# Performance work log

Hardware: AMD Instinct MI355X
Metric: run time of the kernel (lower is better)

The kernel has to match this reference:

```python
import jax, jax.numpy as jnp
import numpy as np

# snntorch default surrogate: ATan with alpha=2.0
@jax.custom_vjp
def spike_fn(x):
    return (x > 0).astype(x.dtype)

def _spike_fwd(x):
    return spike_fn(x), x

def _spike_bwd(x, g):
    alpha = 2.0
    return (g * (alpha / 2.0) / (1.0 + (jnp.pi / 2.0 * alpha * x) ** 2),)

spike_fn.defvjp(_spike_fwd, _spike_bwd)

B, T, D_IN, H, OUT = 256, 25, 768, 2048, 10

def setup_inputs() -> dict:
    key = jax.random.key(0)
    ks = jax.random.split(key, 5)
    def lin(k, fan_in, fan_out):
        bound = 1.0 / np.sqrt(fan_in)
        kw, kb = jax.random.split(k)
        W = jax.random.uniform(kw, (fan_out, fan_in), minval=-bound, maxval=bound, dtype=jnp.float32)
        b = jax.random.uniform(kb, (fan_out,), minval=-bound, maxval=bound, dtype=jnp.float32)
        return W, b
    W1, b1 = lin(ks[0], D_IN, H)
    W2, b2 = lin(ks[1], H, H)
    W3, b3 = lin(ks[2], H, H)
    W4, b4 = lin(ks[3], H, OUT)
    x = jax.random.normal(ks[4], (B, T, D_IN), dtype=jnp.float32)
    beta = jnp.asarray(0.9, jnp.float32)
    thr = jnp.asarray(1.0, jnp.float32)
    return dict(x=x, W1=W1, b1=b1, W2=W2, b2=b2, W3=W3, b3=b3, W4=W4, b4=b4,
                beta1=beta, beta2=beta, beta3=beta, beta4=beta,
                thr1=thr, thr2=thr, thr3=thr, thr4=thr)

def reference(x, W1, b1, W2, b2, W3, b3, W4, b4,
              beta1, beta2, beta3, beta4, thr1, thr2, thr3, thr4):
    # snntorch Leaky (reset_mechanism='subtract', learn_beta, learn_threshold):
    #   reset = detach(heaviside(mem_prev - thr))
    #   mem   = clip(beta,0,1)*mem_prev + cur - reset*thr
    #   spk   = heaviside(mem - thr)   (ATan surrogate in bwd)
    def lif(cur, mem, beta, thr):
        b = jnp.clip(beta, 0.0, 1.0)
        reset = jax.lax.stop_gradient(spike_fn(mem - thr))
        mem = b * mem + cur - reset * thr
        spk = spike_fn(mem - thr)
        return spk, mem

    Bx = x.shape[0]
    def step(carry, x_t):
        m1, m2, m3, m4 = carry
        c1 = x_t @ W1.T + b1; s1, m1 = lif(c1, m1, beta1, thr1)
        c2 = s1 @ W2.T + b2; s2, m2 = lif(c2, m2, beta2, thr2)
        c3 = s2 @ W3.T + b3; s3, m3 = lif(c3, m3, beta3, thr3)
        c4 = s3 @ W4.T + b4; s4, m4 = lif(c4, m4, beta4, thr4)
        return (m1, m2, m3, m4), (s1, s2, s3, s4, m1, m2, m3, m4, c1, c2, c3, c4)

    init = (jnp.zeros((Bx, W1.shape[0]), x.dtype),
            jnp.zeros((Bx, W2.shape[0]), x.dtype),
            jnp.zeros((Bx, W3.shape[0]), x.dtype),
            jnp.zeros((Bx, W4.shape[0]), x.dtype))
    _, recs = jax.lax.scan(step, init, jnp.swapaxes(x, 0, 1))  # time-major scan
    # recs = (spk1..4, mem1..4, cur1..4), each stacked [T, B, feat]
    return recs
```

## Files before the change

kernel.cpp:

```cpp
#include <hip/hip_runtime.h>


typedef int v4i  __attribute__((ext_vector_type(4)));
typedef int v16i __attribute__((ext_vector_type(16)));

#define T_   25
#define BB   256
#define DIN  768
#define HH   2048
#define PT   (BB*HH)
#define PT4  (BB*10)

__global__ __launch_bounds__(256)
void k_decomp_x(const float* __restrict__ x, char* __restrict__ xpl)
{
    int gid = blockIdx.x * 256 + threadIdx.x;
    int r = gid / 48, rem = gid % 48;
    int kc = rem >> 1, h = rem & 1;
    int t = r >> 8, b = r & 255;
    const float* src = x + ((size_t)b * T_ + t) * DIN + kc * 32 + h * 16;
    alignas(16) char dig[4][16];
#pragma unroll
    for (int e = 0; e < 16; ++e) {
        long long V = llround((double)src[e] * 268435456.0);
#pragma unroll
        for (int p = 0; p < 3; ++p) {
            int d = (int)(V & 255); if (d >= 128) d -= 256;
            dig[p][e] = (char)d; V = (V - d) >> 8;
        }
        dig[3][e] = (char)V;
    }
    size_t base = (((size_t)(r >> 5) * 24 + kc) * 4) * 1024 + (size_t)(h * 32 + (r & 31)) * 16;
#pragma unroll
    for (int p = 0; p < 4; ++p)
        *(int4*)(xpl + base + (size_t)p * 1024) = *(const int4*)dig[p];
}

template<int NDIG, int QSH, int KC>
__global__ __launch_bounds__(256)
void k_decomp_w(const float* __restrict__ W, char* __restrict__ wpl, int K)
{
    int gid = blockIdx.x * 256 + threadIdx.x;
    int n = gid / (KC * 2), rem = gid % (KC * 2);
    int kc = rem >> 1, h = rem & 1;
    const float* src = W + (size_t)n * K + kc * 32 + h * 16;
    const double scale = (double)(1ULL << QSH);
    alignas(16) char dig[NDIG][16];
#pragma unroll
    for (int e = 0; e < 16; ++e) {
        long long V = llround((double)src[e] * scale);
#pragma unroll
        for (int p = 0; p < NDIG - 1; ++p) {
            int d = (int)(V & 255); if (d >= 128) d -= 256;
            dig[p][e] = (char)d; V = (V - d) >> 8;
        }
        dig[NDIG - 1][e] = (char)V;
    }
    size_t base = (((size_t)(n >> 5) * KC + kc) * NDIG) * 1024 + (size_t)(h * 32 + (n & 31)) * 16;
#pragma unroll
    for (int p = 0; p < NDIG; ++p)
        *(int4*)(wpl + base + (size_t)p * 1024) = *(const int4*)dig[p];
}

__global__ __launch_bounds__(512)
void k_gemm1(const char* __restrict__ xpl, const char* __restrict__ wpl,
             const float* __restrict__ bias, float* __restrict__ c_out,
             float* __restrict__ res_out)
{
    __shared__ char wlds[32768];
    int tid = threadIdx.x;
    int wm = tid >> 6, l = tid & 63;
    int nt = blockIdx.x;
    int mt = blockIdx.y * 8 + wm;
    v16i acc[5] = {};
    const char* ab = xpl + ((size_t)mt * 24) * 4 * 1024 + (size_t)l * 16;

    for (int kcb = 0; kcb < 3; ++kcb) {
        __syncthreads();
        const char* src = wpl + ((size_t)(nt * 24 + kcb * 8)) * 4 * 1024;
#pragma unroll
        for (int i = 0; i < 4; ++i) {
            int off = tid * 16 + i * 8192;
            *(int4*)(wlds + off) = *(const int4*)(src + off);
        }
        __syncthreads();
#pragma unroll
        for (int kc = 0; kc < 8; ++kc) {
            const char* a8 = ab + (size_t)(kcb * 8 + kc) * 4096;
            const char* w8 = wlds + (size_t)kc * 4096 + (size_t)l * 16;
            v4i xv[4], wv[4];
#pragma unroll
            for (int p = 0; p < 4; ++p) {
                xv[p] = *(const v4i*)(a8 + (size_t)p * 1024);
                wv[p] = *(const v4i*)(w8 + (size_t)p * 1024);
            }
            acc[4] = __builtin_amdgcn_mfma_i32_32x32x32_i8(xv[3], wv[3], acc[4], 0,0,0);
            acc[3] = __builtin_amdgcn_mfma_i32_32x32x32_i8(xv[2], wv[3], acc[3], 0,0,0);
            acc[3] = __builtin_amdgcn_mfma_i32_32x32x32_i8(xv[3], wv[2], acc[3], 0,0,0);
            acc[2] = __builtin_amdgcn_mfma_i32_32x32x32_i8(xv[1], wv[3], acc[2], 0,0,0);
            acc[2] = __builtin_amdgcn_mfma_i32_32x32x32_i8(xv[2], wv[2], acc[2], 0,0,0);
            acc[2] = __builtin_amdgcn_mfma_i32_32x32x32_i8(xv[3], wv[1], acc[2], 0,0,0);
            acc[1] = __builtin_amdgcn_mfma_i32_32x32x32_i8(xv[0], wv[3], acc[1], 0,0,0);
            acc[1] = __builtin_amdgcn_mfma_i32_32x32x32_i8(xv[1], wv[2], acc[1], 0,0,0);
            acc[1] = __builtin_amdgcn_mfma_i32_32x32x32_i8(xv[2], wv[1], acc[1], 0,0,0);
            acc[1] = __builtin_amdgcn_mfma_i32_32x32x32_i8(xv[3], wv[0], acc[1], 0,0,0);
            acc[0] = __builtin_amdgcn_mfma_i32_32x32x32_i8(xv[0], wv[2], acc[0], 0,0,0);
            acc[0] = __builtin_amdgcn_mfma_i32_32x32x32_i8(xv[1], wv[1], acc[0], 0,0,0);
            acc[0] = __builtin_amdgcn_mfma_i32_32x32x32_i8(xv[2], wv[0], acc[0], 0,0,0);
        }
    }
    int half = l >> 5, lr = l & 31;
    int col = nt * 32 + lr;
    double bv = (double)bias[col];
#pragma unroll
    for (int e = 0; e < 16; ++e) {
        int row = (e & 3) + 8 * (e >> 2) + 4 * half;
        int r = mt * 32 + row;
        double hv = (((((double)acc[4][e] * 256.0 + (double)acc[3][e]) * 256.0
                      + (double)acc[2][e]) * 256.0 + (double)acc[1][e]) * 256.0 + (double)acc[0][e]);
        double v = hv * 7.105427357601002e-15 + bv;
        float cf = (float)v;
        float rf = (float)(v - (double)cf);
        size_t off = (size_t)r * HH + col;
        c_out[off] = cf; res_out[off] = rf;
    }
}

__global__ __launch_bounds__(512)
void k_gemm23(const char* __restrict__ aq, const char* __restrict__ wpl,
              const float* __restrict__ bias,
              float* __restrict__ c_out, float* __restrict__ res_out)
{
    __shared__ char wlds[32768];
    int tid = threadIdx.x;
    int wm = tid >> 6, l = tid & 63;
    int half = l >> 5, lr = l & 31;
    int nt = blockIdx.x;
    int mt = blockIdx.y * 8 + wm;
    v16i acc[4] = {};
    const char* ab = aq + (size_t)mt * 65536 + (size_t)l * 16;

    for (int kcb = 0; kcb < 8; ++kcb) {
        __syncthreads();
        const char* src = wpl + ((size_t)(nt * 64 + kcb * 8)) * 4 * 1024;
#pragma unroll
        for (int i = 0; i < 4; ++i) {
            int off = tid * 16 + i * 8192;
            *(int4*)(wlds + off) = *(const int4*)(src + off);
        }
        __syncthreads();
#pragma unroll
        for (int kc = 0; kc < 8; ++kc) {
            v4i a  = *(const v4i*)(ab + (size_t)(kcb * 8 + kc) * 1024);
            const char* w8 = wlds + (size_t)kc * 4096 + (size_t)l * 16;
            v4i w0 = *(const v4i*)(w8);
            v4i w1 = *(const v4i*)(w8 + 1024);
            v4i w2 = *(const v4i*)(w8 + 2048);
            v4i w3 = *(const v4i*)(w8 + 3072);
            acc[0] = __builtin_amdgcn_mfma_i32_32x32x32_i8(a, w0, acc[0], 0,0,0);
            acc[1] = __builtin_amdgcn_mfma_i32_32x32x32_i8(a, w1, acc[1], 0,0,0);
            acc[2] = __builtin_amdgcn_mfma_i32_32x32x32_i8(a, w2, acc[2], 0,0,0);
            acc[3] = __builtin_amdgcn_mfma_i32_32x32x32_i8(a, w3, acc[3], 0,0,0);
        }
    }
    int col = nt * 32 + lr;
    double bv = (double)bias[col];
#pragma unroll
    for (int e = 0; e < 16; ++e) {
        int row = (e & 3) + 8 * (e >> 2) + 4 * half;
        size_t off = (size_t)(mt * 32 + row) * HH + col;
        double dot = ((((double)acc[3][e] * 256.0 + (double)acc[2][e]) * 256.0
                      + (double)acc[1][e]) * 256.0 + (double)acc[0][e]) * 2.9103830456733704e-11;
        double v = dot + bv;
        float cf = (float)v;
        float rf = (float)(v - (double)cf);
        c_out[off] = cf; res_out[off] = rf;
    }
}

template<bool SWZ>
__global__ __launch_bounds__(256)
void k_scan(const float* __restrict__ c, float* __restrict__ res_m,
            float* __restrict__ s, char* __restrict__ sq,
            const float* __restrict__ beta_p, const float* __restrict__ thr_p)
{
    int idx = blockIdx.x * 256 + threadIdx.x;
    int b = idx >> 11, n = idx & 2047;
    double beta = fmin(fmax((double)*beta_p, 0.0), 1.0);
    double thr  = (double)*thr_p;
    double mem = 0.0;
    for (int t = 0; t < T_; ++t) {
        size_t off = (size_t)t * PT + idx;
        double cur = (double)c[off] + (double)res_m[off];
        double reset = (mem > thr) ? 1.0 : 0.0;
        mem = beta * mem + cur - reset * thr;
        bool sp = mem > thr;
        res_m[off] = (float)mem;
        s[off] = sp ? 1.f : 0.f;
        if (SWZ) {
            int r = t * 256 + b;
            size_t sa = ((size_t)((r >> 5) * 64 + (n >> 5))) * 1024
                      + (size_t)((((n >> 4) & 1) * 32 + (r & 31))) * 16 + (n & 15);
            sq[sa] = sp ? 1 : 0;
        }
    }
}

__global__ __launch_bounds__(256)
void k_gemm4(const float* __restrict__ A, const float* __restrict__ W,
             const float* __restrict__ bias,
             float* __restrict__ c_out, float* __restrict__ res_out)
{
    int wid = threadIdx.x >> 6, lane = threadIdx.x & 63;
    int i = blockIdx.x * 4 + wid;
    double a[32];
#pragma unroll
    for (int m = 0; m < 32; ++m)
        a[m] = (double)A[(size_t)i * HH + lane + 64 * m];
    for (int j = 0; j < 10; ++j) {
        double s = 0.0;
#pragma unroll
        for (int m = 0; m < 32; ++m)
            s += a[m] * (double)W[(size_t)j * HH + lane + 64 * m];
#pragma unroll
        for (int o = 32; o > 0; o >>= 1)
            s += __shfl_down(s, o);
        if (lane == 0) {
            double v = s + (double)bias[j];
            float cf = (float)v;
            float rf = (float)(v - (double)cf);
            c_out[i * 10 + j] = cf; res_out[i * 10 + j] = rf;
        }
    }
}

__global__ __launch_bounds__(256)
void k_scan4(const float* __restrict__ c, float* __restrict__ res_m,
             float* __restrict__ s,
             const float* __restrict__ beta_p, const float* __restrict__ thr_p)
{
    int idx = blockIdx.x * 256 + threadIdx.x;
    if (idx >= PT4) return;
    double beta = fmin(fmax((double)*beta_p, 0.0), 1.0);
    double thr  = (double)*thr_p;
    double mem = 0.0;
    for (int t = 0; t < T_; ++t) {
        size_t off = (size_t)t * PT4 + idx;
        double cur = (double)c[off] + (double)res_m[off];
        double reset = (mem > thr) ? 1.0 : 0.0;
        mem = beta * mem + cur - reset * thr;
        res_m[off] = (float)mem;
        s[off] = (mem > thr) ? 1.f : 0.f;
    }
}

#define BM 32
#define BN 64
#define BK 32
__global__ __launch_bounds__(256)
void gemm_lif_f64(const float* __restrict__ A, int lda, const float* __restrict__ W,
                  const float* __restrict__ bias, const double* __restrict__ m64_in,
                  const float* __restrict__ m32_in, double* __restrict__ m64_out,
                  float* __restrict__ cur_out, float* __restrict__ mem_out, float* __restrict__ spk_out,
                  const float* __restrict__ beta_p, const float* __restrict__ thr_p, int K, int N)
{
    __shared__ double As[BK][BM + 4];
    __shared__ double Ws[BK][BN + 4];
    const int tid = threadIdx.x;
    const int bm = blockIdx.y * BM, bn = blockIdx.x * BN;
    const int tx = tid & 15, ty = tid >> 4;
    const int n0 = tx * 4, m0 = ty * 2;
    const int arow = tid >> 3, acol = (tid & 7) * 4;
    double acc[2][4] = {{0,0,0,0},{0,0,0,0}};
    for (int kt = 0; kt < K; kt += BK) {
        float4 av = *reinterpret_cast<const float4*>(A + (size_t)(bm + arow) * lda + kt + acol);
        As[acol+0][arow]=av.x; As[acol+1][arow]=av.y; As[acol+2][arow]=av.z; As[acol+3][arow]=av.w;
#pragma unroll
        for (int r = 0; r < 2; ++r) {
            int n = arow + r * 32;
            float4 wv = *reinterpret_cast<const float4*>(W + (size_t)(bn + n) * K + kt + acol);
            Ws[acol+0][n]=wv.x; Ws[acol+1][n]=wv.y; Ws[acol+2][n]=wv.z; Ws[acol+3][n]=wv.w;
        }
        __syncthreads();
#pragma unroll
        for (int k = 0; k < BK; ++k) {
            double2 a  = *reinterpret_cast<const double2*>(&As[k][m0]);
            double2 w0 = *reinterpret_cast<const double2*>(&Ws[k][n0]);
            double2 w1 = *reinterpret_cast<const double2*>(&Ws[k][n0 + 2]);
            acc[0][0]+=a.x*w0.x; acc[0][1]+=a.x*w0.y; acc[0][2]+=a.x*w1.x; acc[0][3]+=a.x*w1.y;
            acc[1][0]+=a.y*w0.x; acc[1][1]+=a.y*w0.y; acc[1][2]+=a.y*w1.x; acc[1][3]+=a.y*w1.y;
        }
        __syncthreads();
    }
    const double beta = fmin(fmax((double)*beta_p, 0.0), 1.0);
    const double thr  = (double)*thr_p;
#pragma unroll
    for (int r = 0; r < 2; ++r) {
        const size_t off = (size_t)(bm + m0 + r) * N + bn + n0;
        float4 cf, mf, sf;
        float* cfp=&cf.x; float* mfp=&mf.x; float* sfp=&sf.x;
#pragma unroll
        for (int j = 0; j < 4; ++j) {
            double cur = acc[r][j] + (double)bias[bn + n0 + j];
            double mp = m64_in ? m64_in[off + j] : (m32_in ? (double)m32_in[off + j] : 0.0);
            double reset = (mp > thr) ? 1.0 : 0.0;
            double mem = beta * mp + cur - reset * thr;
            cfp[j]=(float)cur; mfp[j]=(float)mem; sfp[j]=(mem > thr)?1.f:0.f;
            if (m64_out) m64_out[off + j] = mem;
        }
        *reinterpret_cast<float4*>(cur_out + off) = cf;
        *reinterpret_cast<float4*>(mem_out + off) = mf;
        *reinterpret_cast<float4*>(spk_out + off) = sf;
    }
}

__global__ __launch_bounds__(256)
void k_fc4_lif(const float* __restrict__ A, const float* __restrict__ W,
               const float* __restrict__ bias, double* __restrict__ m4ws,
               float* __restrict__ c4, float* __restrict__ m4, float* __restrict__ s4,
               const float* __restrict__ beta_p, const float* __restrict__ thr_p, int t0)
{
    int wid = threadIdx.x >> 6, lane = threadIdx.x & 63;
    int i = blockIdx.x * 4 + wid;
    double a[32];
#pragma unroll
    for (int m = 0; m < 32; ++m)
        a[m] = (double)A[(size_t)i * HH + lane + 64 * m];
    double beta = fmin(fmax((double)*beta_p, 0.0), 1.0);
    double thr  = (double)*thr_p;
    for (int j = 0; j < 10; ++j) {
        double s = 0.0;
#pragma unroll
        for (int m = 0; m < 32; ++m)
            s += a[m] * (double)W[(size_t)j * HH + lane + 64 * m];
#pragma unroll
        for (int o = 32; o > 0; o >>= 1)
            s += __shfl_down(s, o);
        if (lane == 0) {
            double cur = s + (double)bias[j];
            double mp = t0 ? 0.0 : m4ws[i * 10 + j];
            double reset = (mp > thr) ? 1.0 : 0.0;
            double mem = beta * mp + cur - reset * thr;
            c4[i * 10 + j] = (float)cur; m4[i * 10 + j] = (float)mem;
            s4[i * 10 + j] = (mem > thr) ? 1.f : 0.f;
            m4ws[i * 10 + j] = mem;
        }
    }
}

extern "C" void kernel_launch(void* const* d_in, const int* in_sizes, int n_in,
                              void* d_out, int out_size, void* d_ws, size_t ws_size,
                              hipStream_t stream) {
    const float* x  = (const float*)d_in[0];
    const float* W1 = (const float*)d_in[1];  const float* b1 = (const float*)d_in[2];
    const float* W2 = (const float*)d_in[3];  const float* b2 = (const float*)d_in[4];
    const float* W3 = (const float*)d_in[5];  const float* b3 = (const float*)d_in[6];
    const float* W4 = (const float*)d_in[7];  const float* b4 = (const float*)d_in[8];
    const float* beta1 = (const float*)d_in[9];  const float* beta2 = (const float*)d_in[10];
    const float* beta3 = (const float*)d_in[11]; const float* beta4 = (const float*)d_in[12];
    const float* thr1 = (const float*)d_in[13];  const float* thr2 = (const float*)d_in[14];
    const float* thr3 = (const float*)d_in[15];  const float* thr4 = (const float*)d_in[16];

    float* out = (float*)d_out;
    const size_t SB = (size_t)T_ * PT, SB4 = (size_t)T_ * PT4;
    float* s1 = out;            float* s2 = out + SB;   float* s3 = out + 2*SB; float* s4 = out + 3*SB;
    float* m1 = s4 + SB4;       float* m2 = m1 + SB;    float* m3 = m1 + 2*SB;  float* m4 = m1 + 3*SB;
    float* c1 = m4 + SB4;       float* c2 = c1 + SB;    float* c3 = c1 + 2*SB;  float* c4 = c1 + 3*SB;

    const size_t XPL = 4ull*6400*768;
    const size_t W1PL = 4ull*2048*768;
    const size_t W23PL = 4ull*2048*2048;
    const size_t SQ = 6400ull*2048;
    size_t need = XPL + W1PL + 2*W23PL + 2*SQ;

    if (ws_size >= need) {
        char* w = (char*)d_ws;
        char* xpl  = w;              char* w1pl = xpl + XPL;
        char* w2pl = w1pl + W1PL;    char* w3pl = w2pl + W23PL;
        char* s1q  = w3pl + W23PL;   char* s2q  = s1q + SQ;

        k_decomp_x<<<1200, 256, 0, stream>>>(x, xpl);
        k_decomp_w<4,35,24><<<384, 256, 0, stream>>>(W1, w1pl, 768);
        k_decomp_w<4,35,64><<<1024, 256, 0, stream>>>(W2, w2pl, 2048);
        k_decomp_w<4,35,64><<<1024, 256, 0, stream>>>(W3, w3pl, 2048);

        k_gemm1<<<dim3(64, 25), 512, 0, stream>>>(xpl, w1pl, b1, c1, m1);
        k_scan<true><<<2048, 256, 0, stream>>>(c1, m1, s1, s1q, beta1, thr1);
        k_gemm23<<<dim3(64, 25), 512, 0, stream>>>(s1q, w2pl, b2, c2, m2);
        k_scan<true><<<2048, 256, 0, stream>>>(c2, m2, s2, s2q, beta2, thr2);
        k_gemm23<<<dim3(64, 25), 512, 0, stream>>>(s2q, w3pl, b3, c3, m3);
        k_scan<false><<<2048, 256, 0, stream>>>(c3, m3, s3, nullptr, beta3, thr3);
        k_gemm4<<<1600, 256, 0, stream>>>(s3, W4, b4, c4, m4);
        k_scan4<<<10, 256, 0, stream>>>(c4, m4, s4, beta4, thr4);
        return;
    }

    const size_t NL = PT;
    const size_t WS_NEED = (3 * NL + PT4) * sizeof(double);
    const bool use64 = (d_ws != nullptr) && (ws_size >= WS_NEED);
    double* wsd = (double*)d_ws;
    double* mm1 = use64 ? wsd : nullptr;
    double* mm2 = use64 ? wsd + NL : nullptr;
    double* mm3 = use64 ? wsd + 2 * NL : nullptr;
    double* mm4 = use64 ? wsd + 3 * NL : nullptr;
    const dim3 grid(HH / BN, BB / BM);
    for (int t = 0; t < T_; ++t) {
        size_t po = (size_t)t * PT, po4 = (size_t)t * PT4;
        gemm_lif_f64<<<grid, 256, 0, stream>>>(x + (size_t)t * DIN, T_ * DIN, W1, b1,
            t ? mm1 : nullptr, t ? m1 + po - PT : nullptr, mm1,
            c1 + po, m1 + po, s1 + po, beta1, thr1, DIN, HH);
        gemm_lif_f64<<<grid, 256, 0, stream>>>(s1 + po, HH, W2, b2,
            t ? mm2 : nullptr, t ? m2 + po - PT : nullptr, mm2,
            c2 + po, m2 + po, s2 + po, beta2, thr2, HH, HH);
        gemm_lif_f64<<<grid, 256, 0, stream>>>(s2 + po, HH, W3, b3,
            t ? mm3 : nullptr, t ? m3 + po - PT : nullptr, mm3,
            c3 + po, m3 + po, s3 + po, beta3, thr3, HH, HH);
        k_fc4_lif<<<64, 256, 0, stream>>>(s3 + po, W4, b4,
            mm4 ? mm4 : (double*)d_ws, c4 + po4, m4 + po4, s4 + po4, beta4, thr4, t == 0);
    }
}
```

Before: 587.9 us.

## Double-buffer weight tiles in gemm23 and move layer-4 GEMM to int8 MFMA

Changes k_gemm23 to double-buffer its LDS weight tiles. The next k-block is loaded into registers while the current one is computed, and one barrier per iteration is removed. Replaces the FP64 layer-4 GEMM with an int8 MFMA kernel that uses swizzled spike planes from the layer-3 scan and a digit-decomposed W4. This adds an extra swizzled output from scan3, a W4 decomposition kernel, and a small-grid GEMM4 that only uses 10 of its 32 output columns.

```diff
diff --git a/kernel.cpp b/kernel.cpp
--- a/kernel.cpp
+++ b/kernel.cpp
@@ -38,10 +38,11 @@
 
 template<int NDIG, int QSH, int KC>
 __global__ __launch_bounds__(256)
-void k_decomp_w(const float* __restrict__ W, char* __restrict__ wpl, int K)
+void k_decomp_w(const float* __restrict__ W, char* __restrict__ wpl, int K, int NROWS)
 {
     int gid = blockIdx.x * 256 + threadIdx.x;
     int n = gid / (KC * 2), rem = gid % (KC * 2);
+    if (n >= NROWS) return;
     int kc = rem >> 1, h = rem & 1;
     const float* src = W + (size_t)n * K + kc * 32 + h * 16;
     const double scale = (double)(1ULL << QSH);
@@ -126,12 +127,12 @@
     }
 }
 
-__global__ __launch_bounds__(512)
+__global__ __launch_bounds__(512, 4)
 void k_gemm23(const char* __restrict__ aq, const char* __restrict__ wpl,
               const float* __restrict__ bias,
               float* __restrict__ c_out, float* __restrict__ res_out)
 {
-    __shared__ char wlds[32768];
+    __shared__ char wlds[2][32768];
     int tid = threadIdx.x;
     int wm = tid >> 6, l = tid & 63;
     int half = l >> 5, lr = l & 31;
@@ -139,20 +140,28 @@
     int mt = blockIdx.y * 8 + wm;
     v16i acc[4] = {};
     const char* ab = aq + (size_t)mt * 65536 + (size_t)l * 16;
+    const char* wsrc = wpl + ((size_t)nt * 64) * 4 * 1024;
+
+    int4 st[4];
+#pragma unroll
+    for (int i = 0; i < 4; ++i)
+        st[i] = *(const int4*)(wsrc + tid * 16 + i * 8192);
+#pragma unroll
+    for (int i = 0; i < 4; ++i)
+        *(int4*)(&wlds[0][tid * 16 + i * 8192]) = st[i];
 
     for (int kcb = 0; kcb < 8; ++kcb) {
+        if (kcb < 7) {
+#pragma unroll
+            for (int i = 0; i < 4; ++i)
+                st[i] = *(const int4*)(wsrc + (size_t)(kcb + 1) * 32768 + tid * 16 + i * 8192);
+        }
         __syncthreads();
-        const char* src = wpl + ((size_t)(nt * 64 + kcb * 8)) * 4 * 1024;
-#pragma unroll
-        for (int i = 0; i < 4; ++i) {
-            int off = tid * 16 + i * 8192;
-            *(int4*)(wlds + off) = *(const int4*)(src + off);
-        }
-        __syncthreads();
+        const char* lbase = wlds[kcb & 1];
 #pragma unroll
         for (int kc = 0; kc < 8; ++kc) {
-            v4i a  = *(const v4i*)(ab + (size_t)(kcb * 8 + kc) * 1024);
-            const char* w8 = wlds + (size_t)kc * 4096 + (size_t)l * 16;
+            v4i a = *(const v4i*)(ab + (size_t)(kcb * 8 + kc) * 1024);
+            const char* w8 = lbase + kc * 4096 + l * 16;
             v4i w0 = *(const v4i*)(w8);
             v4i w1 = *(const v4i*)(w8 + 1024);
             v4i w2 = *(const v4i*)(w8 + 2048);
@@ -161,6 +170,11 @@
             acc[1] = __builtin_amdgcn_mfma_i32_32x32x32_i8(a, w1, acc[1], 0,0,0);
             acc[2] = __builtin_amdgcn_mfma_i32_32x32x32_i8(a, w2, acc[2], 0,0,0);
             acc[3] = __builtin_amdgcn_mfma_i32_32x32x32_i8(a, w3, acc[3], 0,0,0);
+        }
+        if (kcb < 7) {
+#pragma unroll
+            for (int i = 0; i < 4; ++i)
+                *(int4*)(&wlds[(kcb + 1) & 1][tid * 16 + i * 8192]) = st[i];
         }
     }
     int col = nt * 32 + lr;
@@ -206,30 +220,42 @@
     }
 }
 
-__global__ __launch_bounds__(256)
-void k_gemm4(const float* __restrict__ A, const float* __restrict__ W,
-             const float* __restrict__ bias,
-             float* __restrict__ c_out, float* __restrict__ res_out)
-{
-    int wid = threadIdx.x >> 6, lane = threadIdx.x & 63;
-    int i = blockIdx.x * 4 + wid;
-    double a[32];
-#pragma unroll
-    for (int m = 0; m < 32; ++m)
-        a[m] = (double)A[(size_t)i * HH + lane + 64 * m];
-    for (int j = 0; j < 10; ++j) {
-        double s = 0.0;
-#pragma unroll
-        for (int m = 0; m < 32; ++m)
-            s += a[m] * (double)W[(size_t)j * HH + lane + 64 * m];
-#pragma unroll
-        for (int o = 32; o > 0; o >>= 1)
-            s += __shfl_down(s, o);
-        if (lane == 0) {
-            double v = s + (double)bias[j];
+__global__ __launch_bounds__(64)
+void k_gemm4i8(const char* __restrict__ aq, const char* __restrict__ wpl,
+               const float* __restrict__ bias,
+               float* __restrict__ c_out, float* __restrict__ res_out)
+{
+    int l = threadIdx.x;
+    int half = l >> 5, lr = l & 31;
+    int mt = blockIdx.x;
+    v16i acc[4] = {};
+    const char* ab = aq + (size_t)mt * 65536 + (size_t)l * 16;
+    const char* wb = wpl + (size_t)l * 16;
+#pragma unroll 4
+    for (int kc = 0; kc < 64; ++kc) {
+        v4i a = *(const v4i*)(ab + (size_t)kc * 1024);
+        const char* w8 = wb + (size_t)kc * 4096;
+        v4i w0 = *(const v4i*)(w8);
+        v4i w1 = *(const v4i*)(w8 + 1024);
+        v4i w2 = *(const v4i*)(w8 + 2048);
+        v4i w3 = *(const v4i*)(w8 + 3072);
+        acc[0] = __builtin_amdgcn_mfma_i32_32x32x32_i8(a, w0, acc[0], 0,0,0);
+        acc[1] = __builtin_amdgcn_mfma_i32_32x32x32_i8(a, w1, acc[1], 0,0,0);
+        acc[2] = __builtin_amdgcn_mfma_i32_32x32x32_i8(a, w2, acc[2], 0,0,0);
+        acc[3] = __builtin_amdgcn_mfma_i32_32x32x32_i8(a, w3, acc[3], 0,0,0);
+    }
+    if (lr < 10) {
+        double bv = (double)bias[lr];
+#pragma unroll
+        for (int e = 0; e < 16; ++e) {
+            int row = (e & 3) + 8 * (e >> 2) + 4 * half;
+            size_t off = (size_t)(mt * 32 + row) * 10 + lr;
+            double dot = ((((double)acc[3][e] * 256.0 + (double)acc[2][e]) * 256.0
+                          + (double)acc[1][e]) * 256.0 + (double)acc[0][e]) * 2.9103830456733704e-11;
+            double v = dot + bv;
             float cf = (float)v;
             float rf = (float)(v - (double)cf);
-            c_out[i * 10 + j] = cf; res_out[i * 10 + j] = rf;
+            c_out[off] = cf; res_out[off] = rf;
         }
     }
 }
@@ -370,27 +396,31 @@
     const size_t XPL = 4ull*6400*768;
     const size_t W1PL = 4ull*2048*768;
     const size_t W23PL = 4ull*2048*2048;
+    const size_t W4PL = 64ull*4*1024;
     const size_t SQ = 6400ull*2048;
-    size_t need = XPL + W1PL + 2*W23PL + 2*SQ;
+    size_t need = XPL + W1PL + 2*W23PL + 2*SQ + W4PL;
 
     if (ws_size >= need) {
         char* w = (char*)d_ws;
         char* xpl  = w;              char* w1pl = xpl + XPL;
         char* w2pl = w1pl + W1PL;    char* w3pl = w2pl + W23PL;
         char* s1q  = w3pl + W23PL;   char* s2q  = s1q + SQ;
+        char* w4pl = s2q + SQ;
+        char* s3q  = s1q;
 
         k_decomp_x<<<1200, 256, 0, stream>>>(x, xpl);
-        k_decomp_w<4,35,24><<<384, 256, 0, stream>>>(W1, w1pl, 768);
-        k_decomp_w<4,35,64><<<1024, 256, 0, stream>>>(W2, w2pl, 2048);
-        k_decomp_w<4,35,64><<<1024, 256, 0, stream>>>(W3, w3pl, 2048);
+        k_decomp_w<4,35,24><<<384, 256, 0, stream>>>(W1, w1pl, 768, 2048);
+        k_decomp_w<4,35,64><<<1024, 256, 0, stream>>>(W2, w2pl, 2048, 2048);
+        k_decomp_w<4,35,64><<<1024, 256, 0, stream>>>(W3, w3pl, 2048, 2048);
+        k_decomp_w<4,35,64><<<5, 256, 0, stream>>>(W4, w4pl, 2048, 10);
 
         k_gemm1<<<dim3(64, 25), 512, 0, stream>>>(xpl, w1pl, b1, c1, m1);
         k_scan<true><<<2048, 256, 0, stream>>>(c1, m1, s1, s1q, beta1, thr1);
         k_gemm23<<<dim3(64, 25), 512, 0, stream>>>(s1q, w2pl, b2, c2, m2);
         k_scan<true><<<2048, 256, 0, stream>>>(c2, m2, s2, s2q, beta2, thr2);
         k_gemm23<<<dim3(64, 25), 512, 0, stream>>>(s2q, w3pl, b3, c3, m3);
-        k_scan<false><<<2048, 256, 0, stream>>>(c3, m3, s3, nullptr, beta3, thr3);
-        k_gemm4<<<1600, 256, 0, stream>>>(s3, W4, b4, c4, m4);
+        k_scan<true><<<2048, 256, 0, stream>>>(c3, m3, s3, s3q, beta3, thr3);
+        k_gemm4i8<<<200, 64, 0, stream>>>(s3q, w4pl, b4, c4, m4);
         k_scan4<<<10, 256, 0, stream>>>(c4, m4, s4, beta4, thr4);
         return;
     }
```

After: 739.0 us. 1.26x slower.
